# Performance work log

Measured on AMD Instinct MI355X. Metric: run time of the kernel, lower is better.

The kernel has to match this reference:

```python
import jax, jax.numpy as jnp
import numpy as np
from jax import lax

DIM = 192
HEADS = 8
HIDDEN = int(DIM * 2.66)  # 510
EPS_LN = 1e-5
EPS_NORM = 1e-12


def conv1x1(x, w):
    # x: (B,C,H,W), w: (O,I,1,1)
    return lax.conv_general_dilated(x, w, (1, 1), 'VALID',
                                    dimension_numbers=('NCHW', 'OIHW', 'NCHW'))


def dwconv3x3(x, w):
    # depthwise 3x3, padding=1; w: (C,1,3,3)
    c = x.shape[1]
    return lax.conv_general_dilated(x, w, (1, 1), 'SAME',
                                    dimension_numbers=('NCHW', 'OIHW', 'NCHW'),
                                    feature_group_count=c)


def layernorm_chan(x, weight, bias):
    # WithBias LayerNorm over channel dim of NCHW (matches to_3d -> LN(-1) -> to_4d)
    mu = jnp.mean(x, axis=1, keepdims=True)
    var = jnp.var(x, axis=1, keepdims=True)
    xn = (x - mu) * lax.rsqrt(var + EPS_LN)
    return xn * weight[None, :, None, None] + bias[None, :, None, None]


def l2norm(x):
    # F.normalize along last dim with eps=1e-12
    n = jnp.sqrt(jnp.sum(x * x, axis=-1, keepdims=True))
    return x / jnp.maximum(n, EPS_NORM)


def attention(x, temperature, w_qkv, w_qkv_dw, w_proj):
    b, c, h, w = x.shape
    hw = h * w
    head_dim = c // HEADS
    qkv = dwconv3x3(conv1x1(x, w_qkv), w_qkv_dw)  # (B, 3C, H, W)
    q, k, v = jnp.split(qkv, 3, axis=1)
    q = l2norm(q.reshape(b, HEADS, head_dim, hw))
    k = l2norm(k.reshape(b, HEADS, head_dim, hw))
    v = v.reshape(b, HEADS, head_dim, hw)
    # channel-wise attention: (B,H,d,d)
    attn = jnp.einsum('bhde,bhce->bhdc', q, k) * temperature[None]
    attn = jax.nn.softmax(attn, axis=-1)
    out = jnp.einsum('bhdc,bhce->bhde', attn, v).reshape(b, c, h, w)
    return conv1x1(out, w_proj)


def ffn(x, w_in, w_dw, w_out):
    x = conv1x1(x, w_in)                 # (B, 2*hidden, H, W)
    x = dwconv3x3(x, w_dw)
    x1, x2 = jnp.split(x, 2, axis=1)
    x = jax.nn.gelu(x1, approximate=False) * x2
    return conv1x1(x, w_out)


def setup_inputs() -> dict:
    key = jax.random.key(0)
    ks = jax.random.split(key, 8)
    b, c, h, w = 4, DIM, 128, 128
    s = 0.05
    return {
        'x': jax.random.normal(ks[0], (b, c, h, w), jnp.float32),
        'temperature': jnp.ones((HEADS, 1, 1), jnp.float32),
        'ln1_w': jnp.ones((c,), jnp.float32),
        'ln1_b': jnp.zeros((c,), jnp.float32),
        'ln2_w': jnp.ones((c,), jnp.float32),
        'ln2_b': jnp.zeros((c,), jnp.float32),
        'w_qkv': jax.random.normal(ks[1], (3 * c, c, 1, 1), jnp.float32) * s,
        'w_qkv_dw': jax.random.normal(ks[2], (3 * c, 1, 3, 3), jnp.float32) * s,
        'w_proj': jax.random.normal(ks[3], (c, c, 1, 1), jnp.float32) * s,
        'w_in': jax.random.normal(ks[4], (2 * HIDDEN, c, 1, 1), jnp.float32) * s,
        'w_dw': jax.random.normal(ks[5], (2 * HIDDEN, 1, 3, 3), jnp.float32) * s,
        'w_out_ffn': jax.random.normal(ks[6], (c, HIDDEN, 1, 1), jnp.float32) * s,
    }


def reference(x, temperature, ln1_w, ln1_b, ln2_w, ln2_b, w_qkv, w_qkv_dw,
              w_proj, w_in, w_dw, w_out_ffn):
    x = x + attention(layernorm_chan(x, ln1_w, ln1_b), temperature,
                      w_qkv, w_qkv_dw, w_proj)
    x = x + ffn(layernorm_chan(x, ln2_w, ln2_b), w_in, w_dw, w_out_ffn)
    return x
```

## Files before the change

kernel.cpp:

```cpp
#include <hip/hip_runtime.h>
#include <hip/hip_bf16.h>
#include <math.h>


#define HW_ 16384

typedef __attribute__((ext_vector_type(8))) short bf16x8;
typedef __attribute__((ext_vector_type(4))) float f32x4;
typedef __attribute__((ext_vector_type(16))) float f32x16;
typedef __attribute__((ext_vector_type(4))) int i32x4;

union Pack8 { __hip_bfloat16 h[8]; i32x4 v; };

__global__ __launch_bounds__(256) void convert_weights(
    const float* __restrict__ wqkv, const float* __restrict__ wproj,
    const float* __restrict__ win, const float* __restrict__ wout,
    __hip_bfloat16* __restrict__ oq, __hip_bfloat16* __restrict__ op,
    __hip_bfloat16* __restrict__ oi, __hip_bfloat16* __restrict__ oo) {
  const int i = blockIdx.x * 256 + threadIdx.x;
  if (i < 110592) oq[i] = __float2bfloat16(wqkv[i]);
  if (i < 36864)  op[i] = __float2bfloat16(wproj[i]);
  if (i < 196608) {
    int m = i / 192, k = i - m * 192;
    oi[i] = __float2bfloat16(m < 1020 ? win[m * 192 + k] : 0.f);
  }
  if (i < 98304) {
    int m = i >> 9, k = i & 511;
    oo[i] = __float2bfloat16(k < 510 ? wout[m * 510 + k] : 0.f);
  }
}

__global__ __launch_bounds__(256) void ln_t_kernel(
    const float* __restrict__ x, const float* __restrict__ w,
    const float* __restrict__ bi, __hip_bfloat16* __restrict__ yt) {
  const int b = blockIdx.y;
  x += (size_t)b * 192 * HW_;
  yt += (size_t)b * HW_ * 192;
  __shared__ float tile[192][68];
  __shared__ float psum[4][64], psq[4][64];
  __shared__ float mu_s[64], inv_s[64];
  const int tid = threadIdx.x;
  const int p0 = blockIdx.x * 64;
  for (int idx = tid; idx < 192 * 16; idx += 256) {
    int c = idx >> 4, p4 = idx & 15;
    f32x4 v = *(const f32x4*)(x + (size_t)c * HW_ + p0 + p4 * 4);
    *(f32x4*)&tile[c][p4 * 4] = v;
  }
  __syncthreads();
  const int tx = tid & 63, ty = tid >> 6;
  float s = 0.f, s2 = 0.f;
  for (int c = ty * 48; c < ty * 48 + 48; c++) {
    float v = tile[c][tx]; s += v; s2 += v * v;
  }
  psum[ty][tx] = s; psq[ty][tx] = s2;
  __syncthreads();
  if (ty == 0) {
    float ts = psum[0][tx] + psum[1][tx] + psum[2][tx] + psum[3][tx];
    float ts2 = psq[0][tx] + psq[1][tx] + psq[2][tx] + psq[3][tx];
    float mu = ts * (1.f / 192.f);
    float var = ts2 * (1.f / 192.f) - mu * mu;
    mu_s[tx] = mu; inv_s[tx] = rsqrtf(var + 1e-5f);
  }
  __syncthreads();
  for (int idx = tid; idx < 64 * 24; idx += 256) {
    int c8 = idx % 24, p = idx / 24;
    float mu = mu_s[p], inv = inv_s[p];
    Pack8 pk;
    #pragma unroll
    for (int u = 0; u < 8; u++) {
      int c = c8 * 8 + u;
      pk.h[u] = __float2bfloat16((tile[c][p] - mu) * inv * w[c] + bi[c]);
    }
    *(i32x4*)&yt[(size_t)(p0 + p) * 192 + c8 * 8] = pk.v;
  }
}

template <int EPI>
__global__ __launch_bounds__(256) void mfma_gemm(
    const __hip_bfloat16* __restrict__ A, const __hip_bfloat16* __restrict__ Bg,
    const float* __restrict__ Cres, void* __restrict__ Dout,
    int M, int N, int K, size_t Bstr, size_t Cstr, size_t Dstr) {
  const int z = blockIdx.z;
  const __hip_bfloat16* B = Bg + (size_t)z * Bstr;
  const float* C = Cres ? Cres + (size_t)z * Cstr : nullptr;
  __shared__ __align__(16) __hip_bfloat16 As[64][72];
  __shared__ __align__(16) __hip_bfloat16 Bs[128][72];
  const int tid = threadIdx.x;
  const int wave = tid >> 6, lane = tid & 63;
  const int quad = lane >> 4, lr = lane & 15;
  const int wm = (wave & 1) * 32, wn = (wave >> 1) * 64;
  const int row0 = blockIdx.x * 64, col0 = blockIdx.y * 128;

  f32x4 acc[2][4];
  #pragma unroll
  for (int i = 0; i < 2; i++)
    #pragma unroll
    for (int j = 0; j < 4; j++) acc[i][j] = (f32x4){0.f, 0.f, 0.f, 0.f};

  for (int k0 = 0; k0 < K; k0 += 64) {
    #pragma unroll
    for (int l = 0; l < 2; l++) {
      int t = tid + l * 256;
      int row = t >> 3, ch = t & 7;
      i32x4 v = *(const i32x4*)(A + (size_t)(row0 + row) * K + k0 + ch * 8);
      *(i32x4*)&As[row][ch * 8] = v;
    }
    #pragma unroll
    for (int l = 0; l < 4; l++) {
      int t = tid + l * 256;
      int row = t >> 3, ch = t & 7;
      i32x4 v = *(const i32x4*)(B + (size_t)(col0 + row) * K + k0 + ch * 8);
      *(i32x4*)&Bs[row][ch * 8] = v;
    }
    __syncthreads();
    #pragma unroll
    for (int ks = 0; ks < 2; ks++) {
      bf16x8 a0 = *(const bf16x8*)&As[wm + lr][ks * 32 + quad * 8];
      bf16x8 a1 = *(const bf16x8*)&As[wm + 16 + lr][ks * 32 + quad * 8];
      #pragma unroll
      for (int j = 0; j < 4; j++) {
        bf16x8 bb = *(const bf16x8*)&Bs[wn + j * 16 + lr][ks * 32 + quad * 8];
        acc[0][j] = __builtin_amdgcn_mfma_f32_16x16x32_bf16(a0, bb, acc[0][j], 0, 0, 0);
        acc[1][j] = __builtin_amdgcn_mfma_f32_16x16x32_bf16(a1, bb, acc[1][j], 0, 0, 0);
      }
    }
    __syncthreads();
  }

  #pragma unroll
  for (int i = 0; i < 2; i++) {
    #pragma unroll
    for (int r = 0; r < 4; r++) {
      int gm = row0 + wm + i * 16 + quad * 4 + r;
      if (gm >= M) continue;
      #pragma unroll
      for (int j = 0; j < 4; j++) {
        int gn = col0 + wn + j * 16 + lr;
        size_t idx = (size_t)gm * N + gn;
        if (EPI == 0) {
          (((__hip_bfloat16*)Dout) + (size_t)z * Dstr)[idx] = __float2bfloat16(acc[i][j][r]);
        } else {
          (((float*)Dout) + (size_t)z * Dstr)[idx] = acc[i][j][r] + C[idx];
        }
      }
    }
  }
}

__global__ __launch_bounds__(256) void dw_kernel(
    const __hip_bfloat16* __restrict__ in, const float* __restrict__ wdw,
    __hip_bfloat16* __restrict__ out, float* __restrict__ nrm2p) {
  const int b = blockIdx.z;
  in  += (size_t)b * 576 * HW_;
  out += (size_t)b * 576 * HW_;
  const int c = blockIdx.y;
  const int x8 = threadIdx.x & 15;
  const int y = blockIdx.x * 16 + (threadIdx.x >> 4);
  const __hip_bfloat16* ip = in + (size_t)c * HW_;
  const float* wp = wdw + c * 9;
  float wv[9];
  #pragma unroll
  for (int u = 0; u < 9; u++) wv[u] = wp[u];
  float acc[8];
  #pragma unroll
  for (int j = 0; j < 8; j++) acc[j] = 0.f;
  #pragma unroll
  for (int r = 0; r < 3; r++) {
    int yy = y + r - 1;
    if (yy < 0 || yy >= 128) continue;
    const __hip_bfloat16* rp = ip + yy * 128 + x8 * 8;
    Pack8 mid; mid.v = *(const i32x4*)rp;
    float row[10];
    row[0] = (x8 > 0) ? (float)rp[-1] : 0.f;
    #pragma unroll
    for (int u = 0; u < 8; u++) row[1 + u] = (float)mid.h[u];
    row[9] = (x8 < 15) ? (float)rp[8] : 0.f;
    const float wl = wv[r * 3], wc = wv[r * 3 + 1], wr = wv[r * 3 + 2];
    #pragma unroll
    for (int j = 0; j < 8; j++)
      acc[j] += wl * row[j] + wc * row[j + 1] + wr * row[j + 2];
  }
  Pack8 o;
  #pragma unroll
  for (int j = 0; j < 8; j++) o.h[j] = __float2bfloat16(acc[j]);
  *(i32x4*)(out + (size_t)c * HW_ + y * 128 + x8 * 8) = o.v;
  if (c < 384) {
    float s = 0.f;
    #pragma unroll
    for (int j = 0; j < 8; j++) s += acc[j] * acc[j];
    #pragma unroll
    for (int off = 32; off > 0; off >>= 1) s += __shfl_down(s, off, 64);
    __shared__ float wsum[4];
    const int lane = threadIdx.x & 63, wvi = threadIdx.x >> 6;
    if (lane == 0) wsum[wvi] = s;
    __syncthreads();
    if (threadIdx.x == 0)
      nrm2p[((size_t)b * 384 + c) * 8 + blockIdx.x] =
          wsum[0] + wsum[1] + wsum[2] + wsum[3];
  }
}

__global__ __launch_bounds__(256) void gram_kernel(
    const __hip_bfloat16* __restrict__ qkv, float* __restrict__ Gpart) {
  const int b = blockIdx.z;
  qkv   += (size_t)b * 576 * HW_;
  Gpart += (size_t)b * 32 * 8 * 576;
  const int h = blockIdx.x, chunk = blockIdx.y;
  const int tid = threadIdx.x;
  const int w = tid >> 6, lane = tid & 63;
  const int m = lane & 31;
  const int khalf = lane >> 5;
  const __hip_bfloat16* qb = qkv + (size_t)(h * 24) * HW_;
  const __hip_bfloat16* kb = qkv + (size_t)(192 + h * 24) * HW_;
  f32x16 acc;
  #pragma unroll
  for (int i = 0; i < 16; i++) acc[i] = 0.f;
  const int e0 = chunk * 512 + w * 128;
  #pragma unroll
  for (int j = 0; j < 8; j++) {
    const int k0 = e0 + j * 16 + khalf * 8;
    bf16x8 a = *(const bf16x8*)(qb + (size_t)m * HW_ + k0);
    bf16x8 bfr = *(const bf16x8*)(kb + (size_t)m * HW_ + k0);
    acc = __builtin_amdgcn_mfma_f32_32x32x16_bf16(a, bfr, acc, 0, 0, 0);
  }
  __shared__ float gs[4][576];
  #pragma unroll
  for (int r = 0; r < 16; r++) {
    int row = (r & 3) + 8 * (r >> 2) + 4 * khalf;
    if (row < 24 && m < 24) gs[w][row * 24 + m] = acc[r];
  }
  __syncthreads();
  float* gp = Gpart + (size_t)(chunk * 8 + h) * 576;
  for (int t = tid; t < 576; t += 256)
    gp[t] = gs[0][t] + gs[1][t] + gs[2][t] + gs[3][t];
}

__global__ __launch_bounds__(256) void softmax2_kernel(
    const float* __restrict__ Gpart, const float* __restrict__ nrm2p,
    const float* __restrict__ temp, float* __restrict__ P) {
  const int b = blockIdx.y;
  Gpart += (size_t)b * 32 * 8 * 576;
  nrm2p += (size_t)b * 384 * 8;
  P     += (size_t)b * 8 * 576;
  const int h = blockIdx.x;
  const int tid = threadIdx.x;
  __shared__ float Gs[576];
  __shared__ float nq[24], nk[24];
  for (int t = tid; t < 576; t += 256) {
    float s = 0.f;
    for (int ch = 0; ch < 32; ch++)
      s += Gpart[(size_t)(ch * 8 + h) * 576 + t];
    Gs[t] = s;
  }
  if (tid < 48) {
    const int r = (tid < 24) ? (h * 24 + tid) : (192 + h * 24 + tid - 24);
    float s = 0.f;
    #pragma unroll
    for (int j = 0; j < 8; j++) s += nrm2p[(size_t)r * 8 + j];
    float nv = fmaxf(sqrtf(s), 1e-12f);
    if (tid < 24) nq[tid] = nv; else nk[tid - 24] = nv;
  }
  __syncthreads();
  if (tid < 24) {
    const int d = tid;
    const float tp = temp[h];
    float row[24], mx = -1e30f;
    #pragma unroll
    for (int c = 0; c < 24; c++) {
      float v = Gs[d * 24 + c] * tp / (nq[d] * nk[c]);
      row[c] = v; mx = fmaxf(mx, v);
    }
    float s = 0.f;
    #pragma unroll
    for (int c = 0; c < 24; c++) { float e = expf(row[c] - mx); row[c] = e; s += e; }
    const float inv = 1.f / s;
    #pragma unroll
    for (int c = 0; c < 24; c++) P[h * 576 + d * 24 + c] = row[c] * inv;
  }
}

__global__ __launch_bounds__(256) void pv_kernel(
    const float* __restrict__ P, const __hip_bfloat16* __restrict__ qkv,
    __hip_bfloat16* __restrict__ yt) {
  const int b = blockIdx.z;
  P   += (size_t)b * 8 * 576;
  qkv += (size_t)b * 576 * HW_;
  yt  += (size_t)b * HW_ * 192;
  const int hh = blockIdx.x;
  const int e = blockIdx.y * 256 + threadIdx.x;
  __shared__ float Ps[576];
  for (int t = threadIdx.x; t < 576; t += 256) Ps[t] = P[hh * 576 + t];
  __syncthreads();
  const __hip_bfloat16* vb = qkv + (size_t)(384 + hh * 24) * HW_;
  float acc[24];
  #pragma unroll
  for (int d = 0; d < 24; d++) acc[d] = 0.f;
  for (int c = 0; c < 24; c++) {
    float v = (float)vb[(size_t)c * HW_ + e];
    #pragma unroll
    for (int d = 0; d < 24; d++) acc[d] += Ps[d * 24 + c] * v;
  }
  #pragma unroll
  for (int g = 0; g < 3; g++) {
    Pack8 pk;
    #pragma unroll
    for (int u = 0; u < 8; u++) pk.h[u] = __float2bfloat16(acc[g * 8 + u]);
    *(i32x4*)&yt[(size_t)e * 192 + hh * 24 + g * 8] = pk.v;
  }
}

__global__ __launch_bounds__(256) void dwg_t_kernel(
    const __hip_bfloat16* __restrict__ hsrc, const float* __restrict__ wdw,
    __hip_bfloat16* __restrict__ gt, int b0) {
  const int z = blockIdx.z;
  const int bb = b0 + z;
  const int y = blockIdx.x >> 1, xh = blockIdx.x & 1;
  const int cz = blockIdx.y;
  const int tid = threadIdx.x;
  const int cl = tid >> 3, pg = tid & 7;
  const int c = cz * 32 + cl;
  const int px = xh * 64 + pg * 8;
  __shared__ __hip_bfloat16 sg[32][72];
  Pack8 o;
  if (c < 510) {
    const __hip_bfloat16* ha = hsrc + ((size_t)bb * 1024 + c) * HW_;
    const __hip_bfloat16* hb = hsrc + ((size_t)bb * 1024 + c + 510) * HW_;
    const float* wa = wdw + c * 9;
    const float* wb = wdw + (c + 510) * 9;
    float wva[9], wvb[9];
    #pragma unroll
    for (int u = 0; u < 9; u++) { wva[u] = wa[u]; wvb[u] = wb[u]; }
    float s1[8], s2[8];
    #pragma unroll
    for (int j = 0; j < 8; j++) { s1[j] = 0.f; s2[j] = 0.f; }
    #pragma unroll
    for (int r = 0; r < 3; r++) {
      int yy = y + r - 1;
      if (yy < 0 || yy >= 128) continue;
      const int off = yy * 128 + px;
      Pack8 ma; ma.v = *(const i32x4*)(ha + off);
      Pack8 mb; mb.v = *(const i32x4*)(hb + off);
      float rowa[10], rowb[10];
      rowa[0] = (px > 0) ? (float)ha[off - 1] : 0.f;
      rowb[0] = (px > 0) ? (float)hb[off - 1] : 0.f;
      #pragma unroll
      for (int u = 0; u < 8; u++) { rowa[1 + u] = (float)ma.h[u]; rowb[1 + u] = (float)mb.h[u]; }
      rowa[9] = (px < 120) ? (float)ha[off + 8] : 0.f;
      rowb[9] = (px < 120) ? (float)hb[off + 8] : 0.f;
      const float al = wva[r * 3], ac = wva[r * 3 + 1], ar = wva[r * 3 + 2];
      const float bl = wvb[r * 3], bc = wvb[r * 3 + 1], br = wvb[r * 3 + 2];
      #pragma unroll
      for (int j = 0; j < 8; j++) {
        s1[j] += al * rowa[j] + ac * rowa[j + 1] + ar * rowa[j + 2];
        s2[j] += bl * rowb[j] + bc * rowb[j + 1] + br * rowb[j + 2];
      }
    }
    #pragma unroll
    for (int j = 0; j < 8; j++) {
      float ge = 0.5f * s1[j] * (1.f + erff(s1[j] * 0.70710678118654752f));
      o.h[j] = __float2bfloat16(ge * s2[j]);
    }
  } else {
    #pragma unroll
    for (int j = 0; j < 8; j++) o.h[j] = __float2bfloat16(0.f);
  }
  #pragma unroll
  for (int j = 0; j < 8; j++) sg[cl][pg * 8 + j] = o.h[j];
  __syncthreads();
  const int prow = tid >> 2, coff = (tid & 3) * 8;
  Pack8 w8;
  #pragma unroll
  for (int u = 0; u < 8; u++) w8.h[u] = sg[coff + u][prow];
  *(i32x4*)(gt + ((size_t)z * HW_ + y * 128 + xh * 64 + prow) * 512 + cz * 32 + coff) = w8.v;
}

extern "C" void kernel_launch(void* const* d_in, const int* in_sizes, int n_in,
                              void* d_out, int out_size, void* d_ws, size_t ws_size,
                              hipStream_t stream) {
  const float* x     = (const float*)d_in[0];
  const float* temp  = (const float*)d_in[1];
  const float* ln1w  = (const float*)d_in[2];
  const float* ln1b  = (const float*)d_in[3];
  const float* ln2w  = (const float*)d_in[4];
  const float* ln2b  = (const float*)d_in[5];
  const float* wqkv  = (const float*)d_in[6];
  const float* wqkvdw= (const float*)d_in[7];
  const float* wproj = (const float*)d_in[8];
  const float* win   = (const float*)d_in[9];
  const float* wdw   = (const float*)d_in[10];
  const float* wout  = (const float*)d_in[11];
  float* out = (float*)d_out;
  char* ws = (char*)d_ws;

  const int HW = 16384;
  const size_t HWC = (size_t)192 * HW;

  __hip_bfloat16* yt    = (__hip_bfloat16*)(ws + 0);
  __hip_bfloat16* qkva  = (__hip_bfloat16*)(ws + 25165824);
  __hip_bfloat16* qkvb  = (__hip_bfloat16*)(ws + 100663296);
  __hip_bfloat16* hbuf  = (__hip_bfloat16*)(ws + 25165824);
  float*          xa    = (float*)(ws + 176160768);
  __hip_bfloat16* gt    = (__hip_bfloat16*)(ws + 226492416);
  __hip_bfloat16* wqkvB = (__hip_bfloat16*)(ws + 260046848);
  __hip_bfloat16* wprojB= (__hip_bfloat16*)(ws + 260268032);
  __hip_bfloat16* winB  = (__hip_bfloat16*)(ws + 260341760);
  __hip_bfloat16* woutB = (__hip_bfloat16*)(ws + 260734976);
  float*          nrm2p = (float*)(ws + 260931584);
  float*          Gpart = (float*)(ws + 260980736);
  float*          P     = (float*)(ws + 263340032);

  convert_weights<<<768, 256, 0, stream>>>(wqkv, wproj, win, wout,
                                           wqkvB, wprojB, winB, woutB);

  ln_t_kernel<<<dim3(256, 4), 256, 0, stream>>>(x, ln1w, ln1b, yt);
  mfma_gemm<0><<<dim3(9, 128, 4), 256, 0, stream>>>(
      wqkvB, yt, nullptr, qkva, 576, HW, 192,
      (size_t)HW * 192, 0, (size_t)576 * HW);
  dw_kernel<<<dim3(8, 576, 4), 256, 0, stream>>>(qkva, wqkvdw, qkvb, nrm2p);
  gram_kernel<<<dim3(8, 32, 4), 256, 0, stream>>>(qkvb, Gpart);
  softmax2_kernel<<<dim3(8, 4), 256, 0, stream>>>(Gpart, nrm2p, temp, P);
  pv_kernel<<<dim3(8, 64, 4), 256, 0, stream>>>(P, qkvb, yt);
  mfma_gemm<1><<<dim3(3, 128, 4), 256, 0, stream>>>(
      wprojB, yt, x, xa, 192, HW, 192,
      (size_t)HW * 192, HWC, HWC);
  ln_t_kernel<<<dim3(256, 4), 256, 0, stream>>>(xa, ln2w, ln2b, yt);
  mfma_gemm<0><<<dim3(16, 128, 4), 256, 0, stream>>>(
      winB, yt, nullptr, hbuf, 1020, HW, 192,
      (size_t)HW * 192, 0, (size_t)1024 * HW);
  for (int half = 0; half < 2; half++) {
    const int b0 = half * 2;
    dwg_t_kernel<<<dim3(256, 16, 2), 256, 0, stream>>>(hbuf, wdw, gt, b0);
    mfma_gemm<1><<<dim3(3, 128, 2), 256, 0, stream>>>(
        woutB, gt, xa + (size_t)b0 * HWC, out + (size_t)b0 * HWC,
        192, HW, 512, (size_t)HW * 512, HWC, HWC);
  }
}
```

Measured before the change: 559.7 us.

## Process eight output rows per thread in FFN depthwise+GELU kernel to reuse input rows

The depthwise 3x3 + GELU-gating kernel now computes an 8-row strip per block instead of a single row. Each input row is loaded once and accumulated into three rotating row accumulators, which cuts the 3x redundant row reads down to 10/8. Results are staged in a larger shared tile and transposed out eight rows at a time, and the grid shrinks eightfold. In exchange, register pressure rises, shared memory use grows, and there are fewer blocks to hide latency.

```diff
diff --git a/kernel.cpp b/kernel.cpp
--- a/kernel.cpp
+++ b/kernel.cpp
@@ -314,64 +314,89 @@
     __hip_bfloat16* __restrict__ gt, int b0) {
   const int z = blockIdx.z;
   const int bb = b0 + z;
-  const int y = blockIdx.x >> 1, xh = blockIdx.x & 1;
+  const int yt = blockIdx.x >> 1, xh = blockIdx.x & 1;
   const int cz = blockIdx.y;
   const int tid = threadIdx.x;
-  const int cl = tid >> 3, pg = tid & 7;
+  const int cl = tid >> 3, x8 = tid & 7;
   const int c = cz * 32 + cl;
-  const int px = xh * 64 + pg * 8;
-  __shared__ __hip_bfloat16 sg[32][72];
-  Pack8 o;
-  if (c < 510) {
-    const __hip_bfloat16* ha = hsrc + ((size_t)bb * 1024 + c) * HW_;
-    const __hip_bfloat16* hb = hsrc + ((size_t)bb * 1024 + c + 510) * HW_;
-    const float* wa = wdw + c * 9;
-    const float* wb = wdw + (c + 510) * 9;
-    float wva[9], wvb[9];
-    #pragma unroll
-    for (int u = 0; u < 9; u++) { wva[u] = wa[u]; wvb[u] = wb[u]; }
-    float s1[8], s2[8];
-    #pragma unroll
-    for (int j = 0; j < 8; j++) { s1[j] = 0.f; s2[j] = 0.f; }
-    #pragma unroll
-    for (int r = 0; r < 3; r++) {
-      int yy = y + r - 1;
-      if (yy < 0 || yy >= 128) continue;
-      const int off = yy * 128 + px;
+  const int y0 = yt * 8;
+  const int pxb = xh * 64 + x8 * 8;
+  __shared__ __hip_bfloat16 sg[32][522];
+
+  const bool active = (c < 510);
+  const int ca = active ? c : 0;
+  const __hip_bfloat16* ha = hsrc + ((size_t)bb * 1024 + ca) * HW_;
+  const __hip_bfloat16* hb = hsrc + ((size_t)bb * 1024 + ca + 510) * HW_;
+  float wva[9], wvb[9];
+  #pragma unroll
+  for (int u = 0; u < 9; u++) {
+    wva[u] = active ? wdw[c * 9 + u] : 0.f;
+    wvb[u] = active ? wdw[(c + 510) * 9 + u] : 0.f;
+  }
+
+  float aA[3][8], aB[3][8];
+  #pragma unroll
+  for (int s = 0; s < 3; s++)
+    #pragma unroll
+    for (int j = 0; j < 8; j++) { aA[s][j] = 0.f; aB[s][j] = 0.f; }
+
+  #pragma unroll
+  for (int i = 0; i < 10; i++) {
+    const int ry = y0 - 1 + i;
+    float ra[10], rb[10];
+    if (ry >= 0 && ry < 128) {
+      const int off = ry * 128 + pxb;
       Pack8 ma; ma.v = *(const i32x4*)(ha + off);
       Pack8 mb; mb.v = *(const i32x4*)(hb + off);
-      float rowa[10], rowb[10];
-      rowa[0] = (px > 0) ? (float)ha[off - 1] : 0.f;
-      rowb[0] = (px > 0) ? (float)hb[off - 1] : 0.f;
+      ra[0] = (pxb > 0) ? (float)ha[off - 1] : 0.f;
+      rb[0] = (pxb > 0) ? (float)hb[off - 1] : 0.f;
       #pragma unroll
-      for (int u = 0; u < 8; u++) { rowa[1 + u] = (float)ma.h[u]; rowb[1 + u] = (float)mb.h[u]; }
-      rowa[9] = (px < 120) ? (float)ha[off + 8] : 0.f;
-      rowb[9] = (px < 120) ? (float)hb[off + 8] : 0.f;
-      const float al = wva[r * 3], ac = wva[r * 3 + 1], ar = wva[r * 3 + 2];
-      const float bl = wvb[r * 3], bc = wvb[r * 3 + 1], br = wvb[r * 3 + 2];
+      for (int u = 0; u < 8; u++) { ra[1 + u] = (float)ma.h[u]; rb[1 + u] = (float)mb.h[u]; }
+      ra[9] = (pxb < 120) ? (float)ha[off + 8] : 0.f;
+      rb[9] = (pxb < 120) ? (float)hb[off + 8] : 0.f;
+    } else {
+      #pragma unroll
+      for (int u = 0; u < 10; u++) { ra[u] = 0.f; rb[u] = 0.f; }
+    }
+    #pragma unroll
+    for (int r = 0; r < 3; r++) {
+      const int lo = i - r;
+      if (lo < 0 || lo >= 8) continue;
+      const int s = lo % 3;
+      const float a0 = wva[r * 3], a1 = wva[r * 3 + 1], a2 = wva[r * 3 + 2];
+      const float b0w = wvb[r * 3], b1 = wvb[r * 3 + 1], b2 = wvb[r * 3 + 2];
       #pragma unroll
       for (int j = 0; j < 8; j++) {
-        s1[j] += al * rowa[j] + ac * rowa[j + 1] + ar * rowa[j + 2];
-        s2[j] += bl * rowb[j] + bc * rowb[j + 1] + br * rowb[j + 2];
+        aA[s][j] += a0 * ra[j] + a1 * ra[j + 1] + a2 * ra[j + 2];
+        aB[s][j] += b0w * rb[j] + b1 * rb[j + 1] + b2 * rb[j + 2];
       }
     }
-    #pragma unroll
-    for (int j = 0; j < 8; j++) {
-      float ge = 0.5f * s1[j] * (1.f + erff(s1[j] * 0.70710678118654752f));
-      o.h[j] = __float2bfloat16(ge * s2[j]);
-    }
-  } else {
-    #pragma unroll
-    for (int j = 0; j < 8; j++) o.h[j] = __float2bfloat16(0.f);
-  }
-  #pragma unroll
-  for (int j = 0; j < 8; j++) sg[cl][pg * 8 + j] = o.h[j];
-  __syncthreads();
-  const int prow = tid >> 2, coff = (tid & 3) * 8;
-  Pack8 w8;
-  #pragma unroll
-  for (int u = 0; u < 8; u++) w8.h[u] = sg[coff + u][prow];
-  *(i32x4*)(gt + ((size_t)z * HW_ + y * 128 + xh * 64 + prow) * 512 + cz * 32 + coff) = w8.v;
+    {
+      const int lo = i - 2;
+      if (lo >= 0 && lo < 8) {
+        const int s = lo % 3;
+        Pack8 o;
+        #pragma unroll
+        for (int j = 0; j < 8; j++) {
+          float v = aA[s][j];
+          float ge = 0.5f * v * (1.f + erff(v * 0.70710678118654752f));
+          o.h[j] = __float2bfloat16(ge * aB[s][j]);
+          aA[s][j] = 0.f; aB[s][j] = 0.f;
+        }
+        *(i32x4*)&sg[cl][lo * 64 + x8 * 8] = o.v;
+      }
+    }
+  }
+  __syncthreads();
+  const int sp = tid >> 2, ch0 = (tid & 3) * 8;
+  #pragma unroll
+  for (int k = 0; k < 8; k++) {
+    Pack8 o;
+    #pragma unroll
+    for (int u = 0; u < 8; u++) o.h[u] = sg[ch0 + u][k * 64 + sp];
+    const int gp = (y0 + k) * 128 + xh * 64 + sp;
+    *(i32x4*)&gt[((size_t)z * HW_ + gp) * 512 + cz * 32 + ch0] = o.v;
+  }
 }
 
 extern "C" void kernel_launch(void* const* d_in, const int* in_sizes, int n_in,
@@ -429,7 +454,7 @@
       (size_t)HW * 192, 0, (size_t)1024 * HW);
   for (int half = 0; half < 2; half++) {
     const int b0 = half * 2;
-    dwg_t_kernel<<<dim3(256, 16, 2), 256, 0, stream>>>(hbuf, wdw, gt, b0);
+    dwg_t_kernel<<<dim3(32, 16, 2), 256, 0, stream>>>(hbuf, wdw, gt, b0);
     mfma_gemm<1><<<dim3(3, 128, 2), 256, 0, stream>>>(
         woutB, gt, xa + (size_t)b0 * HWC, out + (size_t)b0 * HWC,
         192, HW, 512, (size_t)HW * 512, HWC, HWC);
```

Result: faster. 509.3 us (-9.0%).
